# Performance work log

Hardware: AMD Instinct MI355X
Metric: run time of the kernel (lower is better)

Reference implementation:

```python
import jax, jax.numpy as jnp
import numpy as np

B, S, D = 2, 2048, 1024
H = 16
HD = D // H  # 64
FORESIGHT = -1e9  # masked_fill value for non-causal positions


def setup_inputs() -> dict:
    key = jax.random.key(0)
    ks = jax.random.split(key, 8)
    s = 0.02
    return {
        "x": jax.random.normal(ks[0], (B, S, D), dtype=jnp.float32),
        "Wq": jax.random.normal(ks[1], (D, H * HD), dtype=jnp.float32) * s,
        "bq": jax.random.normal(ks[2], (H * HD,), dtype=jnp.float32) * s,
        "Wk": jax.random.normal(ks[3], (D, H * HD), dtype=jnp.float32) * s,
        "Wv": jax.random.normal(ks[4], (D, H * HD), dtype=jnp.float32) * s,
        "Wo": jax.random.normal(ks[5], (H * HD, D), dtype=jnp.float32) * s,
        "bo": jax.random.normal(ks[6], (D,), dtype=jnp.float32) * s,
    }


def reference(x, Wq, bq, Wk, Wv, Wo, bo):
    b, s, _ = x.shape
    # projections -> [B, H, S, HD]
    q = (x @ Wq + bq).reshape(b, s, H, HD).transpose(0, 2, 1, 3)
    k = (x @ Wk).reshape(b, s, H, HD).transpose(0, 2, 1, 3)
    v = (x @ Wv).reshape(b, s, H, HD).transpose(0, 2, 1, 3)
    # scores [B, H, S, S]
    scores = jnp.einsum("bhqd,bhkd->bhqk", q, k) / jnp.sqrt(jnp.float32(HD))
    # ALiBi bias: slope_h * j (key position), broadcast over queries
    slopes = 2.0 ** (-8.0 * jnp.arange(1, H + 1, dtype=jnp.float32) / H)
    positions = jnp.arange(s, dtype=jnp.float32)
    scores = scores - slopes[None, :, None, None] * positions[None, None, None, :]
    # causal mask: fill strictly-upper triangle with foresight
    causal = jnp.tril(jnp.ones((s, s), dtype=bool))
    scores = jnp.where(causal[None, None, :, :], scores, FORESIGHT)
    attn = jax.nn.softmax(scores, axis=-1)
    out = jnp.einsum("bhqk,bhkd->bhqd", attn, v)
    out = out.transpose(0, 2, 1, 3).reshape(b, s, H * HD)
    return out @ Wo + bo
```

## Files before the change

### kernel.cpp

```cpp
#include <hip/hip_runtime.h>
#include <stdint.h>

#define DDIM 1024
#define HH 16
#define HDIM 64
#define SS 2048

typedef short bf16x8 __attribute__((ext_vector_type(8)));
typedef float f32x4 __attribute__((ext_vector_type(4)));
typedef unsigned short u16;

__device__ __forceinline__ unsigned f2bf(float f) {
  unsigned u = __builtin_bit_cast(unsigned, f);
  u = u + 0x7FFFu + ((u >> 16) & 1u);
  return u >> 16;
}

__device__ __forceinline__ unsigned cvt_pk_bf16(float a, float b) {
  unsigned r;
  asm("v_cvt_pk_bf16_f32 %0, %1, %2" : "=v"(r) : "v"(a), "v"(b));
  return r;
}

__device__ __forceinline__ void gload16(const void* g, void* l) {
  __builtin_amdgcn_global_load_lds(
      (const __attribute__((address_space(1))) unsigned int*)g,
      (__attribute__((address_space(3))) unsigned int*)l, 16, 0, 0);
}

__global__ void k_convert_x(const float* __restrict__ x, u16* __restrict__ xb) {
  int i = (blockIdx.x * 256 + threadIdx.x) * 4;
  float4 v = *(const float4*)(x + i);
  ushort4 o;
  o.x = (u16)f2bf(v.x); o.y = (u16)f2bf(v.y); o.z = (u16)f2bf(v.z); o.w = (u16)f2bf(v.w);
  *(ushort4*)(xb + i) = o;
}

__global__ void k_transpose_w(const float* __restrict__ w0, const float* __restrict__ w1,
                              const float* __restrict__ w2, const float* __restrict__ w3,
                              u16* __restrict__ wt) {
  __shared__ float t[64][65];
  int z = blockIdx.z;
  const float* src = (z == 0) ? w0 : (z == 1) ? w1 : (z == 2) ? w2 : w3;
  u16* dst = wt + (size_t)z * DDIM * DDIM;
  int k0 = blockIdx.x * 64, n0 = blockIdx.y * 64;
  int tid = threadIdx.x;
  int c4 = tid & 15, rr = tid >> 4;
  for (int rep = 0; rep < 4; rep++) {
    int r = rr + rep * 16;
    float4 v = *(const float4*)(src + (size_t)(k0 + r) * DDIM + n0 + c4 * 4);
    t[r][c4 * 4 + 0] = v.x; t[r][c4 * 4 + 1] = v.y;
    t[r][c4 * 4 + 2] = v.z; t[r][c4 * 4 + 3] = v.w;
  }
  __syncthreads();
  for (int rep = 0; rep < 4; rep++) {
    int n = rr + rep * 16;
    ushort4 o;
    o.x = (u16)f2bf(t[c4 * 4 + 0][n]); o.y = (u16)f2bf(t[c4 * 4 + 1][n]);
    o.z = (u16)f2bf(t[c4 * 4 + 2][n]); o.w = (u16)f2bf(t[c4 * 4 + 3][n]);
    *(ushort4*)(dst + (size_t)(n0 + n) * DDIM + k0 + c4 * 4) = o;
  }
}

template <int MODE>
__global__ __launch_bounds__(256, 2) void k_gemm(const u16* __restrict__ A,
                                                 const u16* __restrict__ BT,
                                                 const float* __restrict__ bias,
                                                 void* __restrict__ O0,
                                                 void* __restrict__ O1,
                                                 void* __restrict__ O2) {
  __shared__ __align__(16) u16 lA[128 * 64];
  __shared__ __align__(16) u16 lB[128 * 64];
  const int tid = threadIdx.x;
  const int l = tid & 63, w = tid >> 6;
  const int wm = w >> 1, wn = w & 1;
  const int m0 = blockIdx.x * 128, n0 = blockIdx.y * 128;
  const int lr = l >> 4, lc = l & 15;

  const int srow = l >> 3;
  const int scol = ((l & 7) ^ srow) * 8;

  f32x4 acc[4][4];
  for (int mi = 0; mi < 4; mi++)
    for (int ni = 0; ni < 4; ni++)
      acc[mi][ni] = f32x4{0.f, 0.f, 0.f, 0.f};

  for (int kk = 0; kk < 16; kk++) {
    const int k0 = kk * 64;
    for (int i = 0; i < 4; i++) {
      int c = w * 4 + i;
      gload16(A + (size_t)(m0 + c * 8 + srow) * DDIM + k0 + scol, (char*)lA + c * 1024);
      gload16(BT + (size_t)(n0 + c * 8 + srow) * DDIM + k0 + scol, (char*)lB + c * 1024);
    }
    __syncthreads();
    for (int ks = 0; ks < 2; ks++) {
      bf16x8 af[4], bfr[4];
      for (int mi = 0; mi < 4; mi++) {
        int row = wm * 64 + mi * 16 + lc;
        int slot = (ks * 4 + lr) ^ (row & 7);
        af[mi] = *(const bf16x8*)((const char*)lA + row * 128 + slot * 16);
      }
      for (int ni = 0; ni < 4; ni++) {
        int row = wn * 64 + ni * 16 + lc;
        int slot = (ks * 4 + lr) ^ (row & 7);
        bfr[ni] = *(const bf16x8*)((const char*)lB + row * 128 + slot * 16);
      }
      for (int mi = 0; mi < 4; mi++)
        for (int ni = 0; ni < 4; ni++)
          acc[mi][ni] = __builtin_amdgcn_mfma_f32_16x16x32_bf16(af[mi], bfr[ni], acc[mi][ni], 0, 0, 0);
    }
    __syncthreads();
  }

  if (MODE == 0) {
    const int which = blockIdx.y >> 3;
    if (which == 0) {
      u16* C = (u16*)O0;
      const float c1 = 0.18033688011112043f;
      for (int mi = 0; mi < 4; mi++)
        for (int ni = 0; ni < 4; ni++) {
          int nl = (n0 + wn * 64 + ni * 16 + lc) & 1023;
          float badd = bias[nl];
          for (int r = 0; r < 4; r++) {
            int m = m0 + wm * 64 + mi * 16 + lr * 4 + r;
            C[(size_t)m * DDIM + nl] = (u16)f2bf((acc[mi][ni][r] + badd) * c1);
          }
        }
    } else if (which == 1) {
      u16* C = (u16*)O1;
      for (int mi = 0; mi < 4; mi++)
        for (int ni = 0; ni < 4; ni++) {
          int nl = (n0 + wn * 64 + ni * 16 + lc) & 1023;
          for (int r = 0; r < 4; r++) {
            int m = m0 + wm * 64 + mi * 16 + lr * 4 + r;
            C[(size_t)m * DDIM + nl] = (u16)f2bf(acc[mi][ni][r]);
          }
        }
    } else {
      u16* C = (u16*)O2;
      for (int mi = 0; mi < 4; mi++)
        for (int ni = 0; ni < 4; ni++) {
          int nl = (n0 + wn * 64 + ni * 16 + lc) & 1023;
          int h = nl >> 6, hd = nl & 63;
          int m = m0 + wm * 64 + mi * 16 + lr * 4;
          int b = m >> 11, s = m & 2047;
          unsigned d0 = f2bf(acc[mi][ni][0]) | (f2bf(acc[mi][ni][1]) << 16);
          unsigned d1 = f2bf(acc[mi][ni][2]) | (f2bf(acc[mi][ni][3]) << 16);
          u16* p = C + ((size_t)((b * HH + h) * HDIM + hd)) * SS + s;
          *(unsigned*)(p) = d0;
          *(unsigned*)(p + 2) = d1;
        }
    }
  } else {
    float* C = (float*)O0;
    for (int mi = 0; mi < 4; mi++)
      for (int ni = 0; ni < 4; ni++) {
        int n = n0 + wn * 64 + ni * 16 + lc;
        float badd = bias[n];
        for (int r = 0; r < 4; r++) {
          int m = m0 + wm * 64 + mi * 16 + lr * 4 + r;
          C[(size_t)m * DDIM + n] = acc[mi][ni][r] + badd;
        }
      }
  }
}

__device__ __forceinline__ void attn_tile(int kt, bool masked,
                                          const char* lKc, const char* lVc, char* lPw,
                                          const bf16x8 qf[2], f32x4 of[4],
                                          float& mrun, float& lrun,
                                          float slope2, int lr, int lc, int q_glob) {
  f32x4 sf[4];
#pragma unroll
  for (int kf = 0; kf < 4; kf++) sf[kf] = f32x4{0.f, 0.f, 0.f, 0.f};
  __builtin_amdgcn_s_setprio(1);
#pragma unroll
  for (int ks = 0; ks < 2; ks++)
#pragma unroll
    for (int kf = 0; kf < 4; kf++) {
      int key = kf * 16 + lc;
      int slot = (ks * 4 + lr) ^ (lc & 7);
      bf16x8 a = *(const bf16x8*)(lKc + key * 128 + slot * 16);
      sf[kf] = __builtin_amdgcn_mfma_f32_16x16x32_bf16(a, qf[ks], sf[kf], 0, 0, 0);
    }
  __builtin_amdgcn_s_setprio(0);

  const float base = -slope2 * (float)(kt * 64 + lr * 4);
  float tmax = -3.0e38f;
#pragma unroll
  for (int kf = 0; kf < 4; kf++)
#pragma unroll
    for (int r = 0; r < 4; r++) {
      float sv = sf[kf][r] + (base - slope2 * (float)(kf * 16 + r));
      if (masked) {
        int key = kt * 64 + kf * 16 + lr * 4 + r;
        if (key > q_glob) sv = -3.0e38f;
      }
      sf[kf][r] = sv;
      tmax = fmaxf(tmax, sv);
    }
  tmax = fmaxf(tmax, __shfl_xor(tmax, 16));
  tmax = fmaxf(tmax, __shfl_xor(tmax, 32));

  if (tmax > mrun) {
    float corr = exp2f(mrun - tmax);
    lrun *= corr;
#pragma unroll
    for (int mf = 0; mf < 4; mf++) {
      of[mf][0] *= corr; of[mf][1] *= corr; of[mf][2] *= corr; of[mf][3] *= corr;
    }
    mrun = tmax;
  }

  f32x4 ps = f32x4{0.f, 0.f, 0.f, 0.f};
#pragma unroll
  for (int kf = 0; kf < 4; kf++) {
    float p0 = exp2f(sf[kf][0] - mrun);
    float p1 = exp2f(sf[kf][1] - mrun);
    float p2 = exp2f(sf[kf][2] - mrun);
    float p3 = exp2f(sf[kf][3] - mrun);
    ps[0] += p0; ps[1] += p1; ps[2] += p2; ps[3] += p3;
    uint2 uu;
    uu.x = cvt_pk_bf16(p0, p1);
    uu.y = cvt_pk_bf16(p2, p3);
    int slot = ((kf * 2 + (lr >> 1)) ^ (lc & 7));
    *(uint2*)(lPw + lc * 128 + slot * 16 + (lr & 1) * 8) = uu;
  }
  float psum = (ps[0] + ps[1]) + (ps[2] + ps[3]);
  psum += __shfl_xor(psum, 16);
  psum += __shfl_xor(psum, 32);
  lrun += psum;

  __builtin_amdgcn_s_setprio(1);
#pragma unroll
  for (int ks = 0; ks < 2; ks++) {
    int slotp = (ks * 4 + lr) ^ (lc & 7);
    bf16x8 pb = *(const bf16x8*)(lPw + lc * 128 + slotp * 16);
#pragma unroll
    for (int mf = 0; mf < 4; mf++) {
      int hd = mf * 16 + lc;
      int slotv = (ks * 4 + lr) ^ (lc & 7);
      bf16x8 va = *(const bf16x8*)(lVc + hd * 128 + slotv * 16);
      of[mf] = __builtin_amdgcn_mfma_f32_16x16x32_bf16(va, pb, of[mf], 0, 0, 0);
    }
  }
  __builtin_amdgcn_s_setprio(0);
}

__global__ __launch_bounds__(256, 4) void k_attn(const u16* __restrict__ Q,
                                                 const u16* __restrict__ Kg,
                                                 const u16* __restrict__ Vt,
                                                 u16* __restrict__ AO) {
  __shared__ __align__(16) u16 lK[2][64 * 64];
  __shared__ __align__(16) u16 lV[2][64 * 64];
  __shared__ __align__(16) u16 lP[4][16 * 64];

  const int tid = threadIdx.x;
  const int l = tid & 63, w = tid >> 6;
  const int lr = l >> 4, lc = l & 15;
  const int id = blockIdx.x;
  const int bh = id & 31;
  const int s5 = (id >> 5) & 1;
  const int gg = id >> 6;
  const int qt = s5 ? (31 - gg) : gg;
  const int b = bh >> 4, h = bh & 15;

  const float slope2 = exp2f(-0.5f * (float)(h + 1)) * 1.4426950408889634f;
  const int q_glob = qt * 64 + w * 16 + lc;

  bf16x8 qf[2];
#pragma unroll
  for (int ks = 0; ks < 2; ks++)
    qf[ks] = *(const bf16x8*)(Q + (size_t)(b * SS + q_glob) * DDIM + h * HDIM + ks * 32 + lr * 8);

  f32x4 of[4];
#pragma unroll
  for (int mf = 0; mf < 4; mf++) of[mf] = f32x4{0.f, 0.f, 0.f, 0.f};
  float mrun = -3.0e38f, lrun = 0.f;

  const int srow = l >> 3;
  const int scol = ((l & 7) ^ srow) * 8;
  const int nkt = qt + 1;
  char* lPw = (char*)lP[w];

  auto stage = [&](int kt, int bb) {
#pragma unroll
    for (int i = 0; i < 2; i++) {
      int c = i * 4 + w;
      gload16(Kg + (size_t)(b * SS + kt * 64 + c * 8 + srow) * DDIM + h * HDIM + scol,
              (char*)lK[bb] + c * 1024);
      gload16(Vt + ((size_t)bh * HDIM + c * 8 + srow) * SS + kt * 64 + scol,
              (char*)lV[bb] + c * 1024);
    }
  };

  stage(0, 0);
  asm volatile("s_waitcnt vmcnt(0)" ::: "memory");
  __builtin_amdgcn_s_barrier();
  asm volatile("" ::: "memory");

  for (int kt = 0; kt < nkt - 1; kt++) {
    const int cur = kt & 1;
    stage(kt + 1, cur ^ 1);
    attn_tile(kt, false, (const char*)lK[cur], (const char*)lV[cur], lPw,
              qf, of, mrun, lrun, slope2, lr, lc, q_glob);
    asm volatile("s_waitcnt vmcnt(0)" ::: "memory");
    __builtin_amdgcn_s_barrier();
    asm volatile("" ::: "memory");
  }
  const int cur = (nkt - 1) & 1;
  attn_tile(nkt - 1, true, (const char*)lK[cur], (const char*)lV[cur], lPw,
            qf, of, mrun, lrun, slope2, lr, lc, q_glob);

  float inv = 1.f / lrun;
  u16* obase = AO + (size_t)(b * SS + q_glob) * DDIM + h * HDIM;
#pragma unroll
  for (int mf = 0; mf < 4; mf++) {
    uint2 uu;
    uu.x = cvt_pk_bf16(of[mf][0] * inv, of[mf][1] * inv);
    uu.y = cvt_pk_bf16(of[mf][2] * inv, of[mf][3] * inv);
    *(uint2*)(obase + mf * 16 + lr * 4) = uu;
  }
}

extern "C" void kernel_launch(void* const* d_in, const int* in_sizes, int n_in,
                              void* d_out, int out_size, void* d_ws, size_t ws_size,
                              hipStream_t stream) {
  const float* x  = (const float*)d_in[0];
  const float* Wq = (const float*)d_in[1];
  const float* bq = (const float*)d_in[2];
  const float* Wk = (const float*)d_in[3];
  const float* Wv = (const float*)d_in[4];
  const float* Wo = (const float*)d_in[5];
  const float* bo = (const float*)d_in[6];
  float* out = (float*)d_out;

  u16* ws = (u16*)d_ws;
  const size_t MEG = 1024 * 1024;
  u16* xb = ws;
  u16* WT = ws + 4 * MEG;
  u16* Qb = ws + 8 * MEG;
  u16* Kb = ws + 12 * MEG;
  u16* Vt = ws + 16 * MEG;
  u16* AO = ws + 20 * MEG;

  k_convert_x<<<dim3(4096), dim3(256), 0, stream>>>(x, xb);
  k_transpose_w<<<dim3(16, 16, 4), dim3(256), 0, stream>>>(Wq, Wk, Wv, Wo, WT);
  k_gemm<0><<<dim3(32, 24), dim3(256), 0, stream>>>(xb, WT, bq, (void*)Qb, (void*)Kb, (void*)Vt);
  k_attn<<<dim3(1024), dim3(256), 0, stream>>>(Qb, Kb, Vt, AO);
  k_gemm<1><<<dim3(32, 8), dim3(256), 0, stream>>>(AO, WT + 3 * MEG, bo, (void*)out, nullptr, nullptr);
}
```

Before: 124.5 us.

## Restructure attention to single-wave blocks loading K/V directly into registers

Replaces the 4-wave attention block with shared-memory double-buffered K/V by one-wave blocks that each handle 32 queries (two 16-row fragments). K and V fragments are loaded straight from global memory into registers, with K for the next tile prefetched while the current tile computes. The last diagonal tile skips key fragments that are fully masked. This drops LDS staging and block barriers, but each wave now issues its own global loads with no sharing across waves, and register pressure rises.

New measurement: 162.2 us. 30.3% more time.

```diff
diff --git a/kernel.cpp b/kernel.cpp
--- a/kernel.cpp
+++ b/kernel.cpp
@@ -165,161 +165,177 @@
   }
 }
 
-__device__ __forceinline__ void attn_tile(int kt, bool masked,
-                                          const char* lKc, const char* lVc, char* lPw,
-                                          const bf16x8 qf[2], f32x4 of[4],
-                                          float& mrun, float& lrun,
-                                          float slope2, int lr, int lc, int q_glob) {
-  f32x4 sf[4];
-#pragma unroll
-  for (int kf = 0; kf < 4; kf++) sf[kf] = f32x4{0.f, 0.f, 0.f, 0.f};
-  __builtin_amdgcn_s_setprio(1);
-#pragma unroll
-  for (int ks = 0; ks < 2; ks++)
-#pragma unroll
-    for (int kf = 0; kf < 4; kf++) {
-      int key = kf * 16 + lc;
-      int slot = (ks * 4 + lr) ^ (lc & 7);
-      bf16x8 a = *(const bf16x8*)(lKc + key * 128 + slot * 16);
-      sf[kf] = __builtin_amdgcn_mfma_f32_16x16x32_bf16(a, qf[ks], sf[kf], 0, 0, 0);
-    }
-  __builtin_amdgcn_s_setprio(0);
-
-  const float base = -slope2 * (float)(kt * 64 + lr * 4);
-  float tmax = -3.0e38f;
-#pragma unroll
-  for (int kf = 0; kf < 4; kf++)
-#pragma unroll
-    for (int r = 0; r < 4; r++) {
-      float sv = sf[kf][r] + (base - slope2 * (float)(kf * 16 + r));
-      if (masked) {
-        int key = kt * 64 + kf * 16 + lr * 4 + r;
-        if (key > q_glob) sv = -3.0e38f;
-      }
-      sf[kf][r] = sv;
-      tmax = fmaxf(tmax, sv);
-    }
-  tmax = fmaxf(tmax, __shfl_xor(tmax, 16));
-  tmax = fmaxf(tmax, __shfl_xor(tmax, 32));
-
-  if (tmax > mrun) {
-    float corr = exp2f(mrun - tmax);
-    lrun *= corr;
-#pragma unroll
-    for (int mf = 0; mf < 4; mf++) {
-      of[mf][0] *= corr; of[mf][1] *= corr; of[mf][2] *= corr; of[mf][3] *= corr;
-    }
-    mrun = tmax;
-  }
-
-  f32x4 ps = f32x4{0.f, 0.f, 0.f, 0.f};
-#pragma unroll
-  for (int kf = 0; kf < 4; kf++) {
-    float p0 = exp2f(sf[kf][0] - mrun);
-    float p1 = exp2f(sf[kf][1] - mrun);
-    float p2 = exp2f(sf[kf][2] - mrun);
-    float p3 = exp2f(sf[kf][3] - mrun);
-    ps[0] += p0; ps[1] += p1; ps[2] += p2; ps[3] += p3;
-    uint2 uu;
-    uu.x = cvt_pk_bf16(p0, p1);
-    uu.y = cvt_pk_bf16(p2, p3);
-    int slot = ((kf * 2 + (lr >> 1)) ^ (lc & 7));
-    *(uint2*)(lPw + lc * 128 + slot * 16 + (lr & 1) * 8) = uu;
-  }
-  float psum = (ps[0] + ps[1]) + (ps[2] + ps[3]);
-  psum += __shfl_xor(psum, 16);
-  psum += __shfl_xor(psum, 32);
-  lrun += psum;
-
-  __builtin_amdgcn_s_setprio(1);
-#pragma unroll
-  for (int ks = 0; ks < 2; ks++) {
-    int slotp = (ks * 4 + lr) ^ (lc & 7);
-    bf16x8 pb = *(const bf16x8*)(lPw + lc * 128 + slotp * 16);
-#pragma unroll
-    for (int mf = 0; mf < 4; mf++) {
-      int hd = mf * 16 + lc;
-      int slotv = (ks * 4 + lr) ^ (lc & 7);
-      bf16x8 va = *(const bf16x8*)(lVc + hd * 128 + slotv * 16);
-      of[mf] = __builtin_amdgcn_mfma_f32_16x16x32_bf16(va, pb, of[mf], 0, 0, 0);
-    }
-  }
-  __builtin_amdgcn_s_setprio(0);
-}
-
-__global__ __launch_bounds__(256, 4) void k_attn(const u16* __restrict__ Q,
-                                                 const u16* __restrict__ Kg,
-                                                 const u16* __restrict__ Vt,
-                                                 u16* __restrict__ AO) {
-  __shared__ __align__(16) u16 lK[2][64 * 64];
-  __shared__ __align__(16) u16 lV[2][64 * 64];
-  __shared__ __align__(16) u16 lP[4][16 * 64];
-
-  const int tid = threadIdx.x;
-  const int l = tid & 63, w = tid >> 6;
+__global__ __launch_bounds__(64, 2) void k_attn(const u16* __restrict__ Q,
+                                                const u16* __restrict__ Kg,
+                                                const u16* __restrict__ Vt,
+                                                u16* __restrict__ AO) {
+  __shared__ __align__(16) u16 lP[32 * 64];
+
+  const int l = threadIdx.x;
   const int lr = l >> 4, lc = l & 15;
   const int id = blockIdx.x;
   const int bh = id & 31;
-  const int s5 = (id >> 5) & 1;
-  const int gg = id >> 6;
-  const int qt = s5 ? (31 - gg) : gg;
+  const int j = id >> 5;
+  const int gg = j >> 1;
+  const int qs = (j & 1) ? (63 - gg) : gg;
   const int b = bh >> 4, h = bh & 15;
 
   const float slope2 = exp2f(-0.5f * (float)(h + 1)) * 1.4426950408889634f;
-  const int q_glob = qt * 64 + w * 16 + lc;
-
-  bf16x8 qf[2];
-#pragma unroll
-  for (int ks = 0; ks < 2; ks++)
-    qf[ks] = *(const bf16x8*)(Q + (size_t)(b * SS + q_glob) * DDIM + h * HDIM + ks * 32 + lr * 8);
-
-  f32x4 of[4];
-#pragma unroll
-  for (int mf = 0; mf < 4; mf++) of[mf] = f32x4{0.f, 0.f, 0.f, 0.f};
-  float mrun = -3.0e38f, lrun = 0.f;
-
-  const int srow = l >> 3;
-  const int scol = ((l & 7) ^ srow) * 8;
-  const int nkt = qt + 1;
-  char* lPw = (char*)lP[w];
-
-  auto stage = [&](int kt, int bb) {
-#pragma unroll
-    for (int i = 0; i < 2; i++) {
-      int c = i * 4 + w;
-      gload16(Kg + (size_t)(b * SS + kt * 64 + c * 8 + srow) * DDIM + h * HDIM + scol,
-              (char*)lK[bb] + c * 1024);
-      gload16(Vt + ((size_t)bh * HDIM + c * 8 + srow) * SS + kt * 64 + scol,
-              (char*)lV[bb] + c * 1024);
-    }
+
+  bf16x8 qfr[2][2];
+#pragma unroll
+  for (int qf = 0; qf < 2; qf++)
+#pragma unroll
+    for (int kh = 0; kh < 2; kh++)
+      qfr[qf][kh] = *(const bf16x8*)(Q + (size_t)(b * SS + qs * 32 + qf * 16 + lc) * DDIM +
+                                     h * HDIM + kh * 32 + lr * 8);
+
+  f32x4 of[2][4];
+#pragma unroll
+  for (int qf = 0; qf < 2; qf++)
+#pragma unroll
+    for (int hf = 0; hf < 4; hf++) of[qf][hf] = f32x4{0.f, 0.f, 0.f, 0.f};
+  float mrun[2] = {-3.0e38f, -3.0e38f};
+  float lrun[2] = {0.f, 0.f};
+
+  const int nkt = (qs >> 1) + 1;
+  const u16* Kbase = Kg + (size_t)(b * SS) * DDIM + h * HDIM;
+  const u16* Vbase = Vt + (size_t)bh * HDIM * SS;
+
+  auto loadK = [&](bf16x8 (&kk)[8], int kt) {
+#pragma unroll
+    for (int kf = 0; kf < 4; kf++)
+#pragma unroll
+      for (int kh = 0; kh < 2; kh++)
+        kk[kf * 2 + kh] = *(const bf16x8*)(Kbase + (size_t)(kt * 64 + kf * 16 + lc) * DDIM +
+                                           kh * 32 + lr * 8);
   };
 
-  stage(0, 0);
-  asm volatile("s_waitcnt vmcnt(0)" ::: "memory");
-  __builtin_amdgcn_s_barrier();
-  asm volatile("" ::: "memory");
-
-  for (int kt = 0; kt < nkt - 1; kt++) {
-    const int cur = kt & 1;
-    stage(kt + 1, cur ^ 1);
-    attn_tile(kt, false, (const char*)lK[cur], (const char*)lV[cur], lPw,
-              qf, of, mrun, lrun, slope2, lr, lc, q_glob);
-    asm volatile("s_waitcnt vmcnt(0)" ::: "memory");
-    __builtin_amdgcn_s_barrier();
-    asm volatile("" ::: "memory");
-  }
-  const int cur = (nkt - 1) & 1;
-  attn_tile(nkt - 1, true, (const char*)lK[cur], (const char*)lV[cur], lPw,
-            qf, of, mrun, lrun, slope2, lr, lc, q_glob);
-
-  float inv = 1.f / lrun;
-  u16* obase = AO + (size_t)(b * SS + q_glob) * DDIM + h * HDIM;
-#pragma unroll
-  for (int mf = 0; mf < 4; mf++) {
-    uint2 uu;
-    uu.x = cvt_pk_bf16(of[mf][0] * inv, of[mf][1] * inv);
-    uu.y = cvt_pk_bf16(of[mf][2] * inv, of[mf][3] * inv);
-    *(uint2*)(obase + mf * 16 + lr * 4) = uu;
+  char* lPc = (char*)lP;
+
+  auto tile = [&](bf16x8 (&kc)[8], bf16x8 (&kn)[8], int kt, bool hasnext, bool masked, int kfhi) {
+    bf16x8 vv[8];
+#pragma unroll
+    for (int hf = 0; hf < 4; hf++)
+#pragma unroll
+      for (int ks = 0; ks < 2; ks++)
+        vv[hf * 2 + ks] = *(const bf16x8*)(Vbase + (size_t)(hf * 16 + lc) * SS +
+                                           kt * 64 + ks * 32 + lr * 8);
+    if (hasnext) loadK(kn, kt + 1);
+
+    f32x4 sf[2][4];
+#pragma unroll
+    for (int qf = 0; qf < 2; qf++)
+#pragma unroll
+      for (int kf = 0; kf < 4; kf++) sf[qf][kf] = f32x4{0.f, 0.f, 0.f, 0.f};
+    __builtin_amdgcn_s_setprio(1);
+#pragma unroll
+    for (int kh = 0; kh < 2; kh++)
+#pragma unroll
+      for (int kf = 0; kf < 4; kf++) {
+        if (kf >= kfhi) continue;
+#pragma unroll
+        for (int qf = 0; qf < 2; qf++)
+          sf[qf][kf] = __builtin_amdgcn_mfma_f32_16x16x32_bf16(kc[kf * 2 + kh], qfr[qf][kh],
+                                                               sf[qf][kf], 0, 0, 0);
+      }
+    __builtin_amdgcn_s_setprio(0);
+
+    const float base = -slope2 * (float)(kt * 64 + lr * 4);
+#pragma unroll
+    for (int qf = 0; qf < 2; qf++) {
+      const int q_glob = qs * 32 + qf * 16 + lc;
+      float tmax = -3.0e38f;
+#pragma unroll
+      for (int kf = 0; kf < 4; kf++) {
+        if (kf >= kfhi) continue;
+#pragma unroll
+        for (int r = 0; r < 4; r++) {
+          float sv = sf[qf][kf][r] + (base - slope2 * (float)(kf * 16 + r));
+          if (masked) {
+            int key = kt * 64 + kf * 16 + lr * 4 + r;
+            if (key > q_glob) sv = -3.0e38f;
+          }
+          sf[qf][kf][r] = sv;
+          tmax = fmaxf(tmax, sv);
+        }
+      }
+      tmax = fmaxf(tmax, __shfl_xor(tmax, 16));
+      tmax = fmaxf(tmax, __shfl_xor(tmax, 32));
+      if (tmax > mrun[qf]) {
+        float corr = exp2f(mrun[qf] - tmax);
+        lrun[qf] *= corr;
+#pragma unroll
+        for (int hf = 0; hf < 4; hf++) {
+          of[qf][hf][0] *= corr; of[qf][hf][1] *= corr;
+          of[qf][hf][2] *= corr; of[qf][hf][3] *= corr;
+        }
+        mrun[qf] = tmax;
+      }
+      f32x4 ps = f32x4{0.f, 0.f, 0.f, 0.f};
+#pragma unroll
+      for (int kf = 0; kf < 4; kf++) {
+        if (kf >= kfhi) continue;
+        float p0 = exp2f(sf[qf][kf][0] - mrun[qf]);
+        float p1 = exp2f(sf[qf][kf][1] - mrun[qf]);
+        float p2 = exp2f(sf[qf][kf][2] - mrun[qf]);
+        float p3 = exp2f(sf[qf][kf][3] - mrun[qf]);
+        ps[0] += p0; ps[1] += p1; ps[2] += p2; ps[3] += p3;
+        uint2 uu;
+        uu.x = cvt_pk_bf16(p0, p1);
+        uu.y = cvt_pk_bf16(p2, p3);
+        int slot = (kf * 2 + (lr >> 1)) ^ (lc & 7);
+        *(uint2*)(lPc + (qf * 16 + lc) * 128 + slot * 16 + (lr & 1) * 8) = uu;
+      }
+      float psum = (ps[0] + ps[1]) + (ps[2] + ps[3]);
+      psum += __shfl_xor(psum, 16);
+      psum += __shfl_xor(psum, 32);
+      lrun[qf] += psum;
+    }
+
+    const int kshi = kfhi >> 1;
+    __builtin_amdgcn_s_setprio(1);
+#pragma unroll
+    for (int qf = 0; qf < 2; qf++)
+#pragma unroll
+      for (int ks = 0; ks < 2; ks++) {
+        if (ks >= kshi) continue;
+        int slotp = (ks * 4 + lr) ^ (lc & 7);
+        bf16x8 pb = *(const bf16x8*)(lPc + (qf * 16 + lc) * 128 + slotp * 16);
+#pragma unroll
+        for (int hf = 0; hf < 4; hf++)
+          of[qf][hf] = __builtin_amdgcn_mfma_f32_16x16x32_bf16(vv[hf * 2 + ks], pb,
+                                                               of[qf][hf], 0, 0, 0);
+      }
+    __builtin_amdgcn_s_setprio(0);
+  };
+
+  const int kfhi_last = (qs & 1) ? 4 : 2;
+  bf16x8 ka[8], kb[8];
+  loadK(ka, 0);
+  int kt = 0;
+  for (; kt + 2 <= nkt - 1; kt += 2) {
+    tile(ka, kb, kt, true, false, 4);
+    tile(kb, ka, kt + 1, true, false, 4);
+  }
+  if (kt < nkt - 1) {
+    tile(ka, kb, kt, true, false, 4);
+    tile(kb, ka, nkt - 1, false, true, kfhi_last);
+  } else {
+    tile(ka, kb, nkt - 1, false, true, kfhi_last);
+  }
+
+#pragma unroll
+  for (int qf = 0; qf < 2; qf++) {
+    float inv = 1.f / lrun[qf];
+    u16* obase = AO + (size_t)(b * SS + qs * 32 + qf * 16 + lc) * DDIM + h * HDIM;
+#pragma unroll
+    for (int hf = 0; hf < 4; hf++) {
+      uint2 uu;
+      uu.x = cvt_pk_bf16(of[qf][hf][0] * inv, of[qf][hf][1] * inv);
+      uu.y = cvt_pk_bf16(of[qf][hf][2] * inv, of[qf][hf][3] * inv);
+      *(uint2*)(obase + hf * 16 + lr * 4) = uu;
+    }
   }
 }
 
@@ -347,6 +363,6 @@
   k_convert_x<<<dim3(4096), dim3(256), 0, stream>>>(x, xb);
   k_transpose_w<<<dim3(16, 16, 4), dim3(256), 0, stream>>>(Wq, Wk, Wv, Wo, WT);
   k_gemm<0><<<dim3(32, 24), dim3(256), 0, stream>>>(xb, WT, bq, (void*)Qb, (void*)Kb, (void*)Vt);
-  k_attn<<<dim3(1024), dim3(256), 0, stream>>>(Qb, Kb, Vt, AO);
+  k_attn<<<dim3(2048), dim3(64), 0, stream>>>(Qb, Kb, Vt, AO);
   k_gemm<1><<<dim3(32, 8), dim3(256), 0, stream>>>(AO, WT + 3 * MEG, bo, (void*)out, nullptr, nullptr);
 }
```

## Prefetch two KV tiles ahead, skip masked diagonal MFMAs, defer row-sum reduction

Applied to the files above, without the earlier changes.

The loop now keeps two K/V tiles in flight using a vmcnt(4) wait and a second barrier before refilling a buffer, instead of waiting for all loads each iteration. On the diagonal tile each wave skips the QK and PV MFMA fragments that lie entirely above the causal boundary. The running row-sum is kept per lane and reduced only once at the end, and the max-rescale cross-lane shuffles run only when some lane saw a new maximum. Together these target load latency, wasted masked compute and per-tile shuffle overhead. The trade-off is an extra barrier per tile plus redundant clamped loads issued at the tail.

Result: faster. 121.7 us (-2.3%).

```diff
diff --git a/kernel.cpp b/kernel.cpp
--- a/kernel.cpp
+++ b/kernel.cpp
@@ -165,10 +165,10 @@
   }
 }
 
-__device__ __forceinline__ void attn_tile(int kt, bool masked,
+__device__ __forceinline__ void attn_tile(int kt, bool masked, int kfhi,
                                           const char* lKc, const char* lVc, char* lPw,
                                           const bf16x8 qf[2], f32x4 of[4],
-                                          float& mrun, float& lrun,
+                                          float& mrun, float& lrun_lane,
                                           float slope2, int lr, int lc, int q_glob) {
   f32x4 sf[4];
 #pragma unroll
@@ -178,6 +178,7 @@
   for (int ks = 0; ks < 2; ks++)
 #pragma unroll
     for (int kf = 0; kf < 4; kf++) {
+      if (kf >= kfhi) continue;
       int key = kf * 16 + lc;
       int slot = (ks * 4 + lr) ^ (lc & 7);
       bf16x8 a = *(const bf16x8*)(lKc + key * 128 + slot * 16);
@@ -188,7 +189,8 @@
   const float base = -slope2 * (float)(kt * 64 + lr * 4);
   float tmax = -3.0e38f;
 #pragma unroll
-  for (int kf = 0; kf < 4; kf++)
+  for (int kf = 0; kf < 4; kf++) {
+    if (kf >= kfhi) continue;
 #pragma unroll
     for (int r = 0; r < 4; r++) {
       float sv = sf[kf][r] + (base - slope2 * (float)(kf * 16 + r));
@@ -199,41 +201,49 @@
       sf[kf][r] = sv;
       tmax = fmaxf(tmax, sv);
     }
-  tmax = fmaxf(tmax, __shfl_xor(tmax, 16));
-  tmax = fmaxf(tmax, __shfl_xor(tmax, 32));
-
-  if (tmax > mrun) {
-    float corr = exp2f(mrun - tmax);
-    lrun *= corr;
-#pragma unroll
-    for (int mf = 0; mf < 4; mf++) {
-      of[mf][0] *= corr; of[mf][1] *= corr; of[mf][2] *= corr; of[mf][3] *= corr;
-    }
-    mrun = tmax;
-  }
-
+  }
+
+  if (__any(tmax > mrun)) {
+    float tcol = fmaxf(tmax, __shfl_xor(tmax, 16));
+    tcol = fmaxf(tcol, __shfl_xor(tcol, 32));
+    if (tcol > mrun) {
+      float corr = exp2f(mrun - tcol);
+      lrun_lane *= corr;
+#pragma unroll
+      for (int mf = 0; mf < 4; mf++) {
+        of[mf][0] *= corr; of[mf][1] *= corr; of[mf][2] *= corr; of[mf][3] *= corr;
+      }
+      mrun = tcol;
+    }
+  }
+
+  const int kfUp = (kfhi + 1) & ~1;
   f32x4 ps = f32x4{0.f, 0.f, 0.f, 0.f};
 #pragma unroll
   for (int kf = 0; kf < 4; kf++) {
-    float p0 = exp2f(sf[kf][0] - mrun);
-    float p1 = exp2f(sf[kf][1] - mrun);
-    float p2 = exp2f(sf[kf][2] - mrun);
-    float p3 = exp2f(sf[kf][3] - mrun);
-    ps[0] += p0; ps[1] += p1; ps[2] += p2; ps[3] += p3;
+    if (kf >= kfUp) continue;
     uint2 uu;
-    uu.x = cvt_pk_bf16(p0, p1);
-    uu.y = cvt_pk_bf16(p2, p3);
+    if (kf < kfhi) {
+      float p0 = exp2f(sf[kf][0] - mrun);
+      float p1 = exp2f(sf[kf][1] - mrun);
+      float p2 = exp2f(sf[kf][2] - mrun);
+      float p3 = exp2f(sf[kf][3] - mrun);
+      ps[0] += p0; ps[1] += p1; ps[2] += p2; ps[3] += p3;
+      uu.x = cvt_pk_bf16(p0, p1);
+      uu.y = cvt_pk_bf16(p2, p3);
+    } else {
+      uu.x = 0u; uu.y = 0u;
+    }
     int slot = ((kf * 2 + (lr >> 1)) ^ (lc & 7));
     *(uint2*)(lPw + lc * 128 + slot * 16 + (lr & 1) * 8) = uu;
   }
-  float psum = (ps[0] + ps[1]) + (ps[2] + ps[3]);
-  psum += __shfl_xor(psum, 16);
-  psum += __shfl_xor(psum, 32);
-  lrun += psum;
-
+  lrun_lane += (ps[0] + ps[1]) + (ps[2] + ps[3]);
+
+  const int kshi = kfUp >> 1;
   __builtin_amdgcn_s_setprio(1);
 #pragma unroll
   for (int ks = 0; ks < 2; ks++) {
+    if (ks >= kshi) continue;
     int slotp = (ks * 4 + lr) ^ (lc & 7);
     bf16x8 pb = *(const bf16x8*)(lPw + lc * 128 + slotp * 16);
 #pragma unroll
@@ -276,7 +286,7 @@
   f32x4 of[4];
 #pragma unroll
   for (int mf = 0; mf < 4; mf++) of[mf] = f32x4{0.f, 0.f, 0.f, 0.f};
-  float mrun = -3.0e38f, lrun = 0.f;
+  float mrun = -3.0e38f, lrun_lane = 0.f;
 
   const int srow = l >> 3;
   const int scol = ((l & 7) ^ srow) * 8;
@@ -295,23 +305,26 @@
   };
 
   stage(0, 0);
-  asm volatile("s_waitcnt vmcnt(0)" ::: "memory");
-  __builtin_amdgcn_s_barrier();
-  asm volatile("" ::: "memory");
-
-  for (int kt = 0; kt < nkt - 1; kt++) {
-    const int cur = kt & 1;
-    stage(kt + 1, cur ^ 1);
-    attn_tile(kt, false, (const char*)lK[cur], (const char*)lV[cur], lPw,
-              qf, of, mrun, lrun, slope2, lr, lc, q_glob);
-    asm volatile("s_waitcnt vmcnt(0)" ::: "memory");
+  stage(nkt > 1 ? 1 : 0, 1);
+
+  for (int t = 0; t < nkt; t++) {
+    asm volatile("s_waitcnt vmcnt(4)" ::: "memory");
     __builtin_amdgcn_s_barrier();
     asm volatile("" ::: "memory");
-  }
-  const int cur = (nkt - 1) & 1;
-  attn_tile(nkt - 1, true, (const char*)lK[cur], (const char*)lV[cur], lPw,
-            qf, of, mrun, lrun, slope2, lr, lc, q_glob);
-
+    const bool last = (t == nkt - 1);
+    attn_tile(t, last, last ? (w + 1) : 4,
+              (const char*)lK[t & 1], (const char*)lV[t & 1], lPw,
+              qf, of, mrun, lrun_lane, slope2, lr, lc, q_glob);
+    __builtin_amdgcn_s_barrier();
+    asm volatile("" ::: "memory");
+    int kts = t + 2;
+    if (kts > nkt - 1) kts = nkt - 1;
+    stage(kts, t & 1);
+  }
+
+  float lrun = lrun_lane;
+  lrun += __shfl_xor(lrun, 16);
+  lrun += __shfl_xor(lrun, 32);
   float inv = 1.f / lrun;
   u16* obase = AO + (size_t)(b * SS + q_glob) * DDIM + h * HDIM;
 #pragma unroll
```
